# Kernel optimization log

Measured on AMD Instinct MI355X. Metric: run time of the kernel, lower is better.

Reference implementation:

```python
import jax, jax.numpy as jnp
from jax import lax
import numpy as np


def setup_inputs() -> dict:
    key = jax.random.key(0)
    ks = jax.random.split(key, 7)
    B, T, I, H, O = 8192, 512, 7, 7, 1
    s = 1.0 / np.sqrt(H)
    return {
        "x": jax.random.normal(ks[0], (B, T, I), dtype=jnp.float32),
        "W_ih": jax.random.normal(ks[1], (H, I), dtype=jnp.float32) * s,
        "W_hh": jax.random.normal(ks[2], (H, H), dtype=jnp.float32) * s,
        "b_ih": jax.random.normal(ks[3], (H,), dtype=jnp.float32) * s,
        "b_hh": jax.random.normal(ks[4], (H,), dtype=jnp.float32) * s,
        "W_fc": jax.random.normal(ks[5], (O, H), dtype=jnp.float32) * s,
        "b_fc": jax.random.normal(ks[6], (O,), dtype=jnp.float32) * s,
    }


def reference(x, W_ih, W_hh, b_ih, b_hh, W_fc, b_fc):
    # Vanilla tanh RNN: h_t = tanh(x_t W_ih^T + b_ih + h_{t-1} W_hh^T + b_hh)
    B, T, _ = x.shape
    H = W_hh.shape[0]
    # Precompute the input projection for all timesteps (one big GEMM).
    xp = jnp.einsum("bti,hi->bth", x, W_ih) + (b_ih + b_hh)  # [B,T,H]
    h0 = jnp.zeros((B, H), dtype=x.dtype)

    def step(h, xt):
        h = jnp.tanh(xt + h @ W_hh.T)
        return h, h

    hT, hs = lax.scan(step, h0, jnp.swapaxes(xp, 0, 1))  # hs: [T,B,H]
    out_seq = jnp.swapaxes(hs, 0, 1)  # [B,T,H]
    out = (jnp.einsum("bth,oh->bto", out_seq, W_fc) + b_fc).squeeze(-1)  # [B,T]
    hidden = hT[None]  # [1,B,H] matching torch's (num_layers, B, H)
    return (out, hidden)
```

## Files before the change

### kernel.cpp

```cpp
#include <hip/hip_runtime.h>
#include <stdint.h>


#define B_TOTAL 8192
#define T_STEPS 512

#define DPP_QUAD0 0x00
#define DPP_QUAD1 0x55
#define DPP_QUAD2 0xAA
#define DPP_QUAD3 0xFF
#define DPP_XOR1  0xB1
#define DPP_XOR2  0x4E
#define DPP_HALF_MIRROR 0x141

template <int CTRL>
__device__ __forceinline__ float dpp_mov(float v) {
    int r = __builtin_amdgcn_update_dpp(0, __float_as_int(v), CTRL, 0xF, 0xF, true);
    return __int_as_float(r);
}

__device__ __forceinline__ float tanh_fast(float a) {
    float e = __builtin_amdgcn_exp2f(a * 2.8853900817779268f);
    float r = __builtin_amdgcn_rcpf(e + 1.0f);
    return __builtin_fmaf(-2.0f, r, 1.0f);
}

__global__ __launch_bounds__(64, 1) void rnn_kernel(
    const float* __restrict__ x,
    const float* __restrict__ Wih,
    const float* __restrict__ Whh,
    const float* __restrict__ bih,
    const float* __restrict__ bhh,
    const float* __restrict__ Wfc,
    const float* __restrict__ bfc,
    float* __restrict__ out)
{
    const int tid  = threadIdx.x;
    const int k    = tid & 7;
    const int b    = blockIdx.x * 8 + (tid >> 3);
    const int quad = (tid >> 2) & 1;

    float wih[7];
    float wa[4], wb[4];
    float bias = 0.0f, wfc_own = 0.0f;
    {
        float whh_row[8];
        #pragma unroll
        for (int i = 0; i < 8; ++i) whh_row[i] = 0.0f;
        if (k < 7) {
            #pragma unroll
            for (int i = 0; i < 7; ++i) {
                wih[i] = Wih[k * 7 + i];
                whh_row[i] = Whh[k * 7 + i];
            }
            bias = bih[k] + bhh[k];
            wfc_own = Wfc[k];
        } else {
            #pragma unroll
            for (int i = 0; i < 7; ++i) wih[i] = 0.0f;
        }
        #pragma unroll
        for (int j = 0; j < 4; ++j) {
            wa[j] = quad ? whh_row[4 + j] : whh_row[j];
            wb[j] = quad ? whh_row[j]     : whh_row[4 + j];
        }
    }
    const float bfcv = bfc[0];

    const float4* xrow = (const float4*)(x + (size_t)b * (T_STEPS * 7));
    float* outp = out + (size_t)b * T_STEPS;

    float a0 = 0.f, a1 = 0.f, a2 = 0.f, a3 = 0.f;
    float b0 = 0.f, b1 = 0.f, b2 = 0.f, b3 = 0.f;

    float4 bufA[14], bufB[14];
    #pragma unroll
    for (int i = 0; i < 14; ++i) bufA[i] = xrow[i];

    auto process = [&](const float4 (&buf)[14], int c) {
        float xv[56];
        #pragma unroll
        for (int i = 0; i < 14; ++i) {
            xv[4 * i + 0] = buf[i].x; xv[4 * i + 1] = buf[i].y;
            xv[4 * i + 2] = buf[i].z; xv[4 * i + 3] = buf[i].w;
        }
        float u[8];
        #pragma unroll
        for (int s = 0; s < 8; ++s) {
            const float* xs = &xv[s * 7];
            float p01 = __builtin_fmaf(wih[1], xs[1], wih[0] * xs[0]);
            float p23 = __builtin_fmaf(wih[3], xs[3], wih[2] * xs[2]);
            float p45 = __builtin_fmaf(wih[5], xs[5], wih[4] * xs[4]);
            float p6b = __builtin_fmaf(wih[6], xs[6], bias);
            u[s] = (p01 + p23) + (p45 + p6b);
        }
        float hs[8];
        #pragma unroll
        for (int s = 0; s < 8; ++s) {
            float p0 = __builtin_fmaf(wa[0], a0, u[s]);
            float p1 = __builtin_fmaf(wa[2], a2, wa[1] * a1);
            float p2 = __builtin_fmaf(wb[0], b0, wa[3] * a3);
            float p3 = __builtin_fmaf(wb[2], b2, wb[1] * b1);
            float p4 = wb[3] * b3;
            float acc = (p0 + p1) + (p2 + (p3 + p4));
            float hk = tanh_fast(acc);
            hs[s] = hk;
            a0 = dpp_mov<DPP_QUAD0>(hk);
            a1 = dpp_mov<DPP_QUAD1>(hk);
            a2 = dpp_mov<DPP_QUAD2>(hk);
            a3 = dpp_mov<DPP_QUAD3>(hk);
            b0 = dpp_mov<DPP_HALF_MIRROR>(a0);
            b1 = dpp_mov<DPP_HALF_MIRROR>(a1);
            b2 = dpp_mov<DPP_HALF_MIRROR>(a2);
            b3 = dpp_mov<DPP_HALF_MIRROR>(a3);
        }
        float o[8];
        #pragma unroll
        for (int s = 0; s < 8; ++s) {
            float v = wfc_own * hs[s];
            v += dpp_mov<DPP_XOR1>(v);
            v += dpp_mov<DPP_XOR2>(v);
            v += dpp_mov<DPP_HALF_MIRROR>(v);
            o[s] = v + bfcv;
        }
        if (k == 7) {
            *(float4*)(outp + c * 8 + 0) = make_float4(o[0], o[1], o[2], o[3]);
            *(float4*)(outp + c * 8 + 4) = make_float4(o[4], o[5], o[6], o[7]);
        }
    };

    for (int c = 0; c < 64; c += 2) {
        #pragma unroll
        for (int i = 0; i < 14; ++i) bufB[i] = xrow[(c + 1) * 14 + i];
        process(bufA, c);
        if (c + 2 < 64) {
            #pragma unroll
            for (int i = 0; i < 14; ++i) bufA[i] = xrow[(c + 2) * 14 + i];
        }
        process(bufB, c + 1);
    }

    if (k < 7) {
        int kk = k & 3;
        float hv = (kk == 0) ? a0 : (kk == 1) ? a1 : (kk == 2) ? a2 : a3;
        out[(size_t)B_TOTAL * T_STEPS + (size_t)b * 7 + k] = hv;
    }
}

extern "C" void kernel_launch(void* const* d_in, const int* in_sizes, int n_in,
                              void* d_out, int out_size, void* d_ws, size_t ws_size,
                              hipStream_t stream) {
    const float* x   = (const float*)d_in[0];
    const float* Wih = (const float*)d_in[1];
    const float* Whh = (const float*)d_in[2];
    const float* bih = (const float*)d_in[3];
    const float* bhh = (const float*)d_in[4];
    const float* Wfc = (const float*)d_in[5];
    const float* bfc = (const float*)d_in[6];
    float* out = (float*)d_out;

    rnn_kernel<<<dim3(B_TOTAL / 8), dim3(64), 0, stream>>>(
        x, Wih, Whh, bih, bhh, Wfc, bfc, out);
}
```

Before: 241.2 us.

## Split RNN into recurrence wave and producer wave pipelined through LDS

Uses two waves per block. Wave 0 runs only the serial hidden-state recurrence. Wave 1 loads x, computes the input projection into a double-buffered LDS tile, and reads back the hidden states to compute the FC output. The goal is to take global loads, the projection and the output reduction off the critical recurrence path. In exchange it adds block barriers every chunk and LDS traffic, which may stall the recurrence wave.

```diff
diff --git a/kernel.cpp b/kernel.cpp
--- a/kernel.cpp
+++ b/kernel.cpp
@@ -11,12 +11,12 @@
 #define DPP_QUAD3 0xFF
 #define DPP_XOR1  0xB1
 #define DPP_XOR2  0x4E
-#define DPP_HALF_MIRROR 0x141
+#define DPP_HM    0x141
 
 template <int CTRL>
 __device__ __forceinline__ float dpp_mov(float v) {
-    int r = __builtin_amdgcn_update_dpp(0, __float_as_int(v), CTRL, 0xF, 0xF, true);
-    return __int_as_float(r);
+    int s = __float_as_int(v);
+    return __int_as_float(__builtin_amdgcn_update_dpp(s, s, CTRL, 0xF, 0xF, true));
 }
 
 __device__ __forceinline__ float tanh_fast(float a) {
@@ -25,7 +25,19 @@
     return __builtin_fmaf(-2.0f, r, 1.0f);
 }
 
-__global__ __launch_bounds__(64, 1) void rnn_kernel(
+__device__ __forceinline__ void block_sync() {
+    __asm__ volatile("" ::: "memory");
+    __asm__ volatile("s_waitcnt lgkmcnt(0)" ::: "memory");
+    __builtin_amdgcn_s_barrier();
+    __asm__ volatile("" ::: "memory");
+}
+
+__device__ __forceinline__ float f4c(const float4& v, int c) {
+    switch (c & 3) { case 0: return v.x; case 1: return v.y;
+                     case 2: return v.z; default: return v.w; }
+}
+
+__global__ __launch_bounds__(128, 2) void rnn_kernel(
     const float* __restrict__ x,
     const float* __restrict__ Wih,
     const float* __restrict__ Whh,
@@ -36,114 +48,147 @@
     float* __restrict__ out)
 {
     const int tid  = threadIdx.x;
-    const int k    = tid & 7;
-    const int b    = blockIdx.x * 8 + (tid >> 3);
-    const int quad = (tid >> 2) & 1;
-
-    float wih[7];
-    float wa[4], wb[4];
-    float bias = 0.0f, wfc_own = 0.0f;
-    {
-        float whh_row[8];
-        #pragma unroll
-        for (int i = 0; i < 8; ++i) whh_row[i] = 0.0f;
+    const int wid  = tid >> 6;
+    const int lane = tid & 63;
+    const int k    = lane & 7;
+    const int g    = lane >> 3;
+    const int b    = blockIdx.x * 8 + g;
+    const int quad = (lane >> 2) & 1;
+
+    __shared__ float uBuf[2][8][8][8];
+    __shared__ float hBuf[2][8][8][8];
+
+    const float bfcv = bfc[0];
+    float* outp = out + (size_t)b * T_STEPS;
+
+    if (wid == 0) {
+        float wa[4], wb[4];
+        {
+            float whh_row[8];
+            #pragma unroll
+            for (int i = 0; i < 8; ++i) whh_row[i] = 0.0f;
+            if (k < 7) {
+                #pragma unroll
+                for (int i = 0; i < 7; ++i) whh_row[i] = Whh[k * 7 + i];
+            }
+            #pragma unroll
+            for (int j = 0; j < 4; ++j) {
+                wa[j] = quad ? whh_row[4 + j] : whh_row[j];
+                wb[j] = quad ? whh_row[j]     : whh_row[4 + j];
+            }
+        }
+        float a0 = 0.f, a1 = 0.f, a2 = 0.f, a3 = 0.f;
+        float b0 = 0.f, b1 = 0.f, b2 = 0.f, b3 = 0.f;
+
+        auto w0_chunk = [&](int c) {
+            const float4* up = (const float4*)&uBuf[c & 1][g][k][0];
+            float4 u03 = up[0], u47 = up[1];
+            float us[8] = { u03.x, u03.y, u03.z, u03.w,
+                            u47.x, u47.y, u47.z, u47.w };
+            #pragma unroll
+            for (int s = 0; s < 8; ++s) {
+                float p0 = __builtin_fmaf(wa[0], a0, us[s]);
+                float p1 = __builtin_fmaf(wa[2], a2, wa[1] * a1);
+                float p2 = __builtin_fmaf(wb[0], b0, wa[3] * a3);
+                float p3 = __builtin_fmaf(wb[2], b2, wb[1] * b1);
+                float p4 = wb[3] * b3;
+                float acc = (p0 + p1) + (p2 + (p3 + p4));
+                float hk = tanh_fast(acc);
+                hBuf[c & 1][s][g][k] = hk;
+                a0 = dpp_mov<DPP_QUAD0>(hk);
+                a1 = dpp_mov<DPP_QUAD1>(hk);
+                a2 = dpp_mov<DPP_QUAD2>(hk);
+                a3 = dpp_mov<DPP_QUAD3>(hk);
+                b0 = dpp_mov<DPP_HM>(a0);
+                b1 = dpp_mov<DPP_HM>(a1);
+                b2 = dpp_mov<DPP_HM>(a2);
+                b3 = dpp_mov<DPP_HM>(a3);
+            }
+        };
+
+        block_sync();
+        for (int c = 0; c < 64; c += 2) {
+            w0_chunk(c);
+            block_sync();
+            w0_chunk(c + 1);
+            block_sync();
+        }
         if (k < 7) {
-            #pragma unroll
-            for (int i = 0; i < 7; ++i) {
-                wih[i] = Wih[k * 7 + i];
-                whh_row[i] = Whh[k * 7 + i];
-            }
+            int kk = k & 3;
+            float hv = (kk == 0) ? a0 : (kk == 1) ? a1 : (kk == 2) ? a2 : a3;
+            out[(size_t)B_TOTAL * T_STEPS + (size_t)b * 7 + k] = hv;
+        }
+    } else {
+        float wih[7];
+        float bias = 0.0f, wfc_own = 0.0f;
+        if (k < 7) {
+            #pragma unroll
+            for (int i = 0; i < 7; ++i) wih[i] = Wih[k * 7 + i];
             bias = bih[k] + bhh[k];
             wfc_own = Wfc[k];
         } else {
             #pragma unroll
             for (int i = 0; i < 7; ++i) wih[i] = 0.0f;
         }
-        #pragma unroll
-        for (int j = 0; j < 4; ++j) {
-            wa[j] = quad ? whh_row[4 + j] : whh_row[j];
-            wb[j] = quad ? whh_row[j]     : whh_row[4 + j];
-        }
-    }
-    const float bfcv = bfc[0];
-
-    const float4* xrow = (const float4*)(x + (size_t)b * (T_STEPS * 7));
-    float* outp = out + (size_t)b * T_STEPS;
-
-    float a0 = 0.f, a1 = 0.f, a2 = 0.f, a3 = 0.f;
-    float b0 = 0.f, b1 = 0.f, b2 = 0.f, b3 = 0.f;
-
-    float4 bufA[14], bufB[14];
-    #pragma unroll
-    for (int i = 0; i < 14; ++i) bufA[i] = xrow[i];
-
-    auto process = [&](const float4 (&buf)[14], int c) {
-        float xv[56];
-        #pragma unroll
-        for (int i = 0; i < 14; ++i) {
-            xv[4 * i + 0] = buf[i].x; xv[4 * i + 1] = buf[i].y;
-            xv[4 * i + 2] = buf[i].z; xv[4 * i + 3] = buf[i].w;
-        }
-        float u[8];
-        #pragma unroll
-        for (int s = 0; s < 8; ++s) {
-            const float* xs = &xv[s * 7];
-            float p01 = __builtin_fmaf(wih[1], xs[1], wih[0] * xs[0]);
-            float p23 = __builtin_fmaf(wih[3], xs[3], wih[2] * xs[2]);
-            float p45 = __builtin_fmaf(wih[5], xs[5], wih[4] * xs[4]);
-            float p6b = __builtin_fmaf(wih[6], xs[6], bias);
-            u[s] = (p01 + p23) + (p45 + p6b);
-        }
-        float hs[8];
-        #pragma unroll
-        for (int s = 0; s < 8; ++s) {
-            float p0 = __builtin_fmaf(wa[0], a0, u[s]);
-            float p1 = __builtin_fmaf(wa[2], a2, wa[1] * a1);
-            float p2 = __builtin_fmaf(wb[0], b0, wa[3] * a3);
-            float p3 = __builtin_fmaf(wb[2], b2, wb[1] * b1);
-            float p4 = wb[3] * b3;
-            float acc = (p0 + p1) + (p2 + (p3 + p4));
-            float hk = tanh_fast(acc);
-            hs[s] = hk;
-            a0 = dpp_mov<DPP_QUAD0>(hk);
-            a1 = dpp_mov<DPP_QUAD1>(hk);
-            a2 = dpp_mov<DPP_QUAD2>(hk);
-            a3 = dpp_mov<DPP_QUAD3>(hk);
-            b0 = dpp_mov<DPP_HALF_MIRROR>(a0);
-            b1 = dpp_mov<DPP_HALF_MIRROR>(a1);
-            b2 = dpp_mov<DPP_HALF_MIRROR>(a2);
-            b3 = dpp_mov<DPP_HALF_MIRROR>(a3);
-        }
-        float o[8];
-        #pragma unroll
-        for (int s = 0; s < 8; ++s) {
-            float v = wfc_own * hs[s];
-            v += dpp_mov<DPP_XOR1>(v);
-            v += dpp_mov<DPP_XOR2>(v);
-            v += dpp_mov<DPP_HALF_MIRROR>(v);
-            o[s] = v + bfcv;
-        }
-        if (k == 7) {
-            *(float4*)(outp + c * 8 + 0) = make_float4(o[0], o[1], o[2], o[3]);
-            *(float4*)(outp + c * 8 + 4) = make_float4(o[4], o[5], o[6], o[7]);
-        }
-    };
-
-    for (int c = 0; c < 64; c += 2) {
-        #pragma unroll
-        for (int i = 0; i < 14; ++i) bufB[i] = xrow[(c + 1) * 14 + i];
-        process(bufA, c);
-        if (c + 2 < 64) {
-            #pragma unroll
-            for (int i = 0; i < 14; ++i) bufA[i] = xrow[(c + 2) * 14 + i];
-        }
-        process(bufB, c + 1);
-    }
-
-    if (k < 7) {
-        int kk = k & 3;
-        float hv = (kk == 0) ? a0 : (kk == 1) ? a1 : (kk == 2) ? a2 : a3;
-        out[(size_t)B_TOTAL * T_STEPS + (size_t)b * 7 + k] = hv;
+
+        const float4* xrow = (const float4*)(x + (size_t)b * (T_STEPS * 7));
+        float4 bufA[14], bufB[14];
+
+        auto w1_load = [&](float4 (&buf)[14], int ch) {
+            const float4* src = xrow + ch * 14;
+            #pragma unroll
+            for (int i = 0; i < 14; ++i) buf[i] = src[i];
+        };
+        auto w1_u = [&](const float4 (&buf)[14], int cn) {
+            float us[8];
+            #pragma unroll
+            for (int s = 0; s < 8; ++s) {
+                float acc = bias;
+                #pragma unroll
+                for (int i = 0; i < 7; ++i)
+                    acc = __builtin_fmaf(wih[i], f4c(buf[(s * 7 + i) >> 2], s * 7 + i), acc);
+                us[s] = acc;
+            }
+            float4* dst = (float4*)&uBuf[cn & 1][g][k][0];
+            dst[0] = make_float4(us[0], us[1], us[2], us[3]);
+            dst[1] = make_float4(us[4], us[5], us[6], us[7]);
+        };
+        auto w1_fly = [&](int cp) {
+            float hs[8];
+            #pragma unroll
+            for (int s = 0; s < 8; ++s) hs[s] = hBuf[cp & 1][s][g][k];
+            float o[8];
+            #pragma unroll
+            for (int s = 0; s < 8; ++s) {
+                float v = wfc_own * hs[s];
+                v += dpp_mov<DPP_XOR1>(v);
+                v += dpp_mov<DPP_XOR2>(v);
+                v += dpp_mov<DPP_HM>(v);
+                o[s] = v + bfcv;
+            }
+            if (k == 7) {
+                *(float4*)(outp + cp * 8 + 0) = make_float4(o[0], o[1], o[2], o[3]);
+                *(float4*)(outp + cp * 8 + 4) = make_float4(o[4], o[5], o[6], o[7]);
+            }
+        };
+
+        w1_load(bufA, 0);
+        w1_load(bufB, 1);
+        w1_u(bufA, 0);
+        w1_load(bufA, 2);
+        block_sync();
+
+        for (int c = 0; c < 64; c += 2) {
+            w1_u(bufB, c + 1);
+            if (c + 3 < 64) w1_load(bufB, c + 3);
+            if (c > 0) w1_fly(c - 1);
+            block_sync();
+            if (c + 2 < 64) w1_u(bufA, c + 2);
+            if (c + 4 < 64) w1_load(bufA, c + 4);
+            w1_fly(c);
+            block_sync();
+        }
+        w1_fly(63);
     }
 }
 
@@ -159,6 +204,6 @@
     const float* bfc = (const float*)d_in[6];
     float* out = (float*)d_out;
 
-    rnn_kernel<<<dim3(B_TOTAL / 8), dim3(64), 0, stream>>>(
+    rnn_kernel<<<dim3(B_TOTAL / 8), dim3(128), 0, stream>>>(
         x, Wih, Whh, bih, bhh, Wfc, bfc, out);
 }
```

Result: faster. 230.5 us (-4.4%).

## Use inline-asm async x loads with explicit vmcnt waits and 256-thread blocks

Applied to the files above, without the earlier changes.

Replaces the compiler-managed double-buffered x loads with hand-issued global_load_dwordx4 inline asm and explicit s_waitcnt vmcnt waits. Each buffer is refilled right after its input projection is done, so loads overlap the serial recurrence. Blocks grow from 64 to 256 threads, which gives 256 blocks instead of 1024. Counting vmcnt by hand is fragile because the output stores may also count against it and change the wait semantics. The larger blocks also change how waves are spread across CUs.

```diff
diff --git a/kernel.cpp b/kernel.cpp
--- a/kernel.cpp
+++ b/kernel.cpp
@@ -11,12 +11,12 @@
 #define DPP_QUAD3 0xFF
 #define DPP_XOR1  0xB1
 #define DPP_XOR2  0x4E
-#define DPP_HALF_MIRROR 0x141
+#define DPP_HM    0x141
 
 template <int CTRL>
 __device__ __forceinline__ float dpp_mov(float v) {
-    int r = __builtin_amdgcn_update_dpp(0, __float_as_int(v), CTRL, 0xF, 0xF, true);
-    return __int_as_float(r);
+    int s = __float_as_int(v);
+    return __int_as_float(__builtin_amdgcn_update_dpp(s, s, CTRL, 0xF, 0xF, true));
 }
 
 __device__ __forceinline__ float tanh_fast(float a) {
@@ -25,7 +25,25 @@
     return __builtin_fmaf(-2.0f, r, 1.0f);
 }
 
-__global__ __launch_bounds__(64, 1) void rnn_kernel(
+typedef float v4f __attribute__((ext_vector_type(4)));
+
+struct XChunk { v4f v[14]; };
+
+__device__ __forceinline__ void chunk_issue(XChunk& ch, const float* base) {
+    #pragma unroll
+    for (int i = 0; i < 14; ++i)
+        asm volatile("global_load_dwordx4 %0, %1, off offset:%2"
+                     : "=v"(ch.v[i]) : "v"(base), "i"(16 * i));
+}
+
+#define CHUNK_WAIT(ch, N)                                                     \
+    asm volatile("s_waitcnt vmcnt(" #N ")"                                    \
+        : "+v"((ch).v[0]), "+v"((ch).v[1]), "+v"((ch).v[2]), "+v"((ch).v[3]), \
+          "+v"((ch).v[4]), "+v"((ch).v[5]), "+v"((ch).v[6]), "+v"((ch).v[7]), \
+          "+v"((ch).v[8]), "+v"((ch).v[9]), "+v"((ch).v[10]),                 \
+          "+v"((ch).v[11]), "+v"((ch).v[12]), "+v"((ch).v[13]))
+
+__global__ __launch_bounds__(256, 1) void rnn_kernel(
     const float* __restrict__ x,
     const float* __restrict__ Wih,
     const float* __restrict__ Whh,
@@ -37,7 +55,7 @@
 {
     const int tid  = threadIdx.x;
     const int k    = tid & 7;
-    const int b    = blockIdx.x * 8 + (tid >> 3);
+    const int b    = blockIdx.x * 32 + (tid >> 3);
     const int quad = (tid >> 2) & 1;
 
     float wih[7];
@@ -67,33 +85,36 @@
     }
     const float bfcv = bfc[0];
 
-    const float4* xrow = (const float4*)(x + (size_t)b * (T_STEPS * 7));
+    const float* xrow = x + (size_t)b * (T_STEPS * 7);
     float* outp = out + (size_t)b * T_STEPS;
 
     float a0 = 0.f, a1 = 0.f, a2 = 0.f, a3 = 0.f;
     float b0 = 0.f, b1 = 0.f, b2 = 0.f, b3 = 0.f;
 
-    float4 bufA[14], bufB[14];
-    #pragma unroll
-    for (int i = 0; i < 14; ++i) bufA[i] = xrow[i];
+    XChunk A, B;
+    chunk_issue(A, xrow);
+    chunk_issue(B, xrow + 56);
 
-    auto process = [&](const float4 (&buf)[14], int c) {
-        float xv[56];
-        #pragma unroll
-        for (int i = 0; i < 14; ++i) {
-            xv[4 * i + 0] = buf[i].x; xv[4 * i + 1] = buf[i].y;
-            xv[4 * i + 2] = buf[i].z; xv[4 * i + 3] = buf[i].w;
+    auto do_chunk = [&](XChunk& buf, int c, const float* reload) {
+        float u[8];
+        {
+            float xv[56];
+            #pragma unroll
+            for (int i = 0; i < 14; ++i) {
+                xv[4 * i + 0] = buf.v[i].x; xv[4 * i + 1] = buf.v[i].y;
+                xv[4 * i + 2] = buf.v[i].z; xv[4 * i + 3] = buf.v[i].w;
+            }
+            #pragma unroll
+            for (int s = 0; s < 8; ++s) {
+                const float* xs = &xv[s * 7];
+                float p01 = __builtin_fmaf(wih[1], xs[1], wih[0] * xs[0]);
+                float p23 = __builtin_fmaf(wih[3], xs[3], wih[2] * xs[2]);
+                float p45 = __builtin_fmaf(wih[5], xs[5], wih[4] * xs[4]);
+                float p6b = __builtin_fmaf(wih[6], xs[6], bias);
+                u[s] = (p01 + p23) + (p45 + p6b);
+            }
         }
-        float u[8];
-        #pragma unroll
-        for (int s = 0; s < 8; ++s) {
-            const float* xs = &xv[s * 7];
-            float p01 = __builtin_fmaf(wih[1], xs[1], wih[0] * xs[0]);
-            float p23 = __builtin_fmaf(wih[3], xs[3], wih[2] * xs[2]);
-            float p45 = __builtin_fmaf(wih[5], xs[5], wih[4] * xs[4]);
-            float p6b = __builtin_fmaf(wih[6], xs[6], bias);
-            u[s] = (p01 + p23) + (p45 + p6b);
-        }
+        if (reload) chunk_issue(buf, reload);
         float hs[8];
         #pragma unroll
         for (int s = 0; s < 8; ++s) {
@@ -109,10 +130,10 @@
             a1 = dpp_mov<DPP_QUAD1>(hk);
             a2 = dpp_mov<DPP_QUAD2>(hk);
             a3 = dpp_mov<DPP_QUAD3>(hk);
-            b0 = dpp_mov<DPP_HALF_MIRROR>(a0);
-            b1 = dpp_mov<DPP_HALF_MIRROR>(a1);
-            b2 = dpp_mov<DPP_HALF_MIRROR>(a2);
-            b3 = dpp_mov<DPP_HALF_MIRROR>(a3);
+            b0 = dpp_mov<DPP_HM>(a0);
+            b1 = dpp_mov<DPP_HM>(a1);
+            b2 = dpp_mov<DPP_HM>(a2);
+            b3 = dpp_mov<DPP_HM>(a3);
         }
         float o[8];
         #pragma unroll
@@ -120,7 +141,7 @@
             float v = wfc_own * hs[s];
             v += dpp_mov<DPP_XOR1>(v);
             v += dpp_mov<DPP_XOR2>(v);
-            v += dpp_mov<DPP_HALF_MIRROR>(v);
+            v += dpp_mov<DPP_HM>(v);
             o[s] = v + bfcv;
         }
         if (k == 7) {
@@ -129,16 +150,17 @@
         }
     };
 
-    for (int c = 0; c < 64; c += 2) {
-        #pragma unroll
-        for (int i = 0; i < 14; ++i) bufB[i] = xrow[(c + 1) * 14 + i];
-        process(bufA, c);
-        if (c + 2 < 64) {
-            #pragma unroll
-            for (int i = 0; i < 14; ++i) bufA[i] = xrow[(c + 2) * 14 + i];
-        }
-        process(bufB, c + 1);
+    #pragma unroll 1
+    for (int c = 0; c < 62; c += 2) {
+        CHUNK_WAIT(A, 14);
+        do_chunk(A, c, xrow + (c + 2) * 56);
+        CHUNK_WAIT(B, 14);
+        do_chunk(B, c + 1, xrow + (c + 3) * 56);
     }
+    CHUNK_WAIT(A, 14);
+    do_chunk(A, 62, nullptr);
+    CHUNK_WAIT(B, 0);
+    do_chunk(B, 63, nullptr);
 
     if (k < 7) {
         int kk = k & 3;
@@ -159,6 +181,6 @@
     const float* bfc = (const float*)d_in[6];
     float* out = (float*)d_out;
 
-    rnn_kernel<<<dim3(B_TOTAL / 8), dim3(64), 0, stream>>>(
+    rnn_kernel<<<dim3(B_TOTAL / 32), dim3(256), 0, stream>>>(
         x, Wih, Whh, bih, bhh, Wfc, bfc, out);
 }
```

Result: faster. 203.3 us (-15.7%).
